# Kernel optimization log

Hardware: AMD Instinct MI355X
Metric: run time of the kernel (lower is better)

Reference implementation:

```python
import jax, jax.numpy as jnp
import numpy as np

NEG_INF = -1e9


def setup_inputs() -> dict:
    key0 = jax.random.key(0)
    ks = jax.random.split(key0, 7)
    B, Tq, Tv, D, U = 8, 512, 512, 512, 128
    query = jax.random.normal(ks[0], (B, Tq, D), dtype=jnp.float32)
    key = jax.random.normal(ks[1], (B, Tv, D), dtype=jnp.float32)
    value = jax.random.normal(ks[2], (B, Tv, D), dtype=jnp.float32)
    mask = jax.random.randint(ks[3], (B, Tv), 0, 2).astype(bool)
    mask = mask.at[:, 0].set(True)  # ensure no fully-masked row
    Wa = jax.random.normal(ks[4], (D, U), dtype=jnp.float32) * (1.0 / np.sqrt(D))
    Ua = jax.random.normal(ks[5], (D, U), dtype=jnp.float32) * (1.0 / np.sqrt(D))
    scale = jax.random.normal(ks[6], (U,), dtype=jnp.float32) * 0.1
    return {"query": query, "key": key, "value": value, "mask": mask,
            "Wa": Wa, "Ua": Ua, "scale": scale}


def reference(query, key, value, mask, Wa, Ua, scale):
    # Dense projections (no bias)
    q = query @ Wa          # [B, Tq, U]
    k = key @ Ua            # [B, Tv, U]
    # Additive (Bahdanau) scores with learned per-unit scale:
    # scores[b,i,j] = sum_u scale[u] * tanh(q[b,i,u] + k[b,j,u])
    t = jnp.tanh(q[:, :, None, :] + k[:, None, :, :])   # [B, Tq, Tv, U]
    scores = jnp.einsum('bijU,U->bij', t, scale)         # [B, Tq, Tv]
    # Mask padded keys/values then softmax over Tv
    scores = jnp.where(mask[:, None, :], scores, NEG_INF)
    weights = jax.nn.softmax(scores, axis=-1)            # [B, Tq, Tv]
    # Weighted sum of values (query_mask is all-True in source -> no-op)
    context = jnp.einsum('bij,bjd->bid', weights, value) # [B, Tq, D]
    return context
```

## Files before the change

### kernel.cpp

```cpp
#include <hip/hip_runtime.h>

constexpr int Bb = 8;
constexpr int Tq = 512;
constexpr int Tv = 512;
constexpr int Dd = 512;
constexpr int Uu = 128;
constexpr float C2LOG2E = 2.88539008177792681f;
constexpr float LOG2E   = 1.44269504088896341f;

__global__ __launch_bounds__(512, 8) void proj_kernel(
    const float* __restrict__ query,
    const float* __restrict__ key,
    const float* __restrict__ Wa,
    const float* __restrict__ Ua,
    const int* __restrict__ mask,
    float* __restrict__ qf2, float* __restrict__ kT)
{
    const int R    = blockIdx.x * 8;
    const bool isQ = R < Bb * Tq;
    const float* __restrict__ src = isQ ? query : key;
    const float* __restrict__ W   = isQ ? Wa : Ua;
    const int Rloc = isQ ? R : R - Bb * Tq;

    __shared__ float smem[8 * 8 * 128];
    __shared__ int posLoc[8];
    float* __restrict__ x = smem;
    const int t = threadIdx.x;

    {
        const float4* __restrict__ s4 =
            reinterpret_cast<const float4*>(src + (size_t)Rloc * Dd);
        float4* x4 = reinterpret_cast<float4*>(x);
#pragma unroll
        for (int m = 0; m < 2; ++m) x4[t + 512 * m] = s4[t + 512 * m];
    }
    if (!isQ && t < 64) {
        const int b  = Rloc >> 9;
        const int j0 = Rloc & 511;
        int base = 0;
#pragma unroll
        for (int c = 0; c < 8; ++c) {
            const int j = c * 64 + t;
            const int v = (mask[b * 512 + j] != 0);
            const unsigned long long bits = __ballot(v);
            const int pos = base + (int)__popcll(bits & ((1ull << t) - 1ull));
            if (j >= j0 && j < j0 + 8) posLoc[j - j0] = v ? pos : -1;
            base += (int)__popcll(bits);
        }
    }
    __syncthreads();

    const int ub = t & 63;
    const int dq = t >> 6;
    const float* __restrict__ Wq = W + (size_t)dq * 64 * Uu;
    const float* __restrict__ xq = x + dq * 64;

    float acc[8][2];
#pragma unroll
    for (int r = 0; r < 8; ++r) { acc[r][0] = 0.f; acc[r][1] = 0.f; }

#pragma unroll 2
    for (int d4 = 0; d4 < 16; ++d4) {
        const int d = d4 * 4;
        const float w0x = Wq[(d + 0) * Uu + ub], w1x = Wq[(d + 0) * Uu + ub + 64];
        const float w0y = Wq[(d + 1) * Uu + ub], w1y = Wq[(d + 1) * Uu + ub + 64];
        const float w0z = Wq[(d + 2) * Uu + ub], w1z = Wq[(d + 2) * Uu + ub + 64];
        const float w0w = Wq[(d + 3) * Uu + ub], w1w = Wq[(d + 3) * Uu + ub + 64];
#pragma unroll
        for (int r = 0; r < 8; ++r) {
            const float4 xv = *reinterpret_cast<const float4*>(xq + r * Dd + d);
            acc[r][0] = fmaf(xv.x, w0x, acc[r][0]);
            acc[r][0] = fmaf(xv.y, w0y, acc[r][0]);
            acc[r][0] = fmaf(xv.z, w0z, acc[r][0]);
            acc[r][0] = fmaf(xv.w, w0w, acc[r][0]);
            acc[r][1] = fmaf(xv.x, w1x, acc[r][1]);
            acc[r][1] = fmaf(xv.y, w1y, acc[r][1]);
            acc[r][1] = fmaf(xv.z, w1z, acc[r][1]);
            acc[r][1] = fmaf(xv.w, w1w, acc[r][1]);
        }
    }

    __syncthreads();
    {
        float* __restrict__ part = smem;
#pragma unroll
        for (int r = 0; r < 8; ++r) {
            part[(dq * 8 + r) * 128 + ub]      = acc[r][0];
            part[(dq * 8 + r) * 128 + ub + 64] = acc[r][1];
        }
    }
    __syncthreads();

    {
        const float* __restrict__ part = smem;
        const int r  = t >> 6;
        const int u0 = (t & 63) * 2;
        float s0 = 0.f, s1 = 0.f;
#pragma unroll
        for (int p = 0; p < 8; ++p) {
            const float2 pv = *reinterpret_cast<const float2*>(part + (p * 8 + r) * 128 + u0);
            s0 += pv.x;
            s1 += pv.y;
        }
        float2 e;
        e.x = __builtin_amdgcn_exp2f(C2LOG2E * s0);
        e.y = __builtin_amdgcn_exp2f(C2LOG2E * s1);
        if (isQ) {
            *reinterpret_cast<float2*>(qf2 + (size_t)(Rloc + r) * Uu + u0) = e;
        } else {
            const int p = posLoc[r];
            if (p >= 0) {
                float* __restrict__ kb = kT + (size_t)(Rloc >> 9) * Uu * Tv;
                const int u4 = u0 >> 2;
                const int c  = u0 & 3;
                *reinterpret_cast<float2*>(kb + ((size_t)u4 * Tv + p) * 4 + c) = e;
            }
        }
    }
}

__global__ __launch_bounds__(512, 8) void attn_kernel(
    const float* __restrict__ qf2, const float* __restrict__ kT,
    const float* __restrict__ value,
    const int* __restrict__ mask,
    const float* __restrict__ scale,
    float* __restrict__ out)
{
    const int bid = blockIdx.x;
    const int swz = (bid & 7) * 128 + (bid >> 3);
    const int r0 = swz * 4;
    const int b  = r0 >> 9;
    const int t  = threadIdx.x;

    __shared__ float q2[4 * Uu];
    __shared__ float s2[Uu];
    __shared__ int   jl[Tv];
    __shared__ float w[4 * Tv];
    __shared__ float pbuf[4 * Tv];
    __shared__ float inv4[4];
    __shared__ int   cntS;

    jl[t] = 0;
    if (t < 128)
        reinterpret_cast<float4*>(q2)[t] =
            reinterpret_cast<const float4*>(qf2 + (size_t)r0 * Uu)[t];
    else if (t < 256) s2[t - 128] = scale[t - 128];
    __syncthreads();
    if (t < 64) {
        int base = 0;
#pragma unroll
        for (int c = 0; c < 8; ++c) {
            const int j = c * 64 + t;
            const int v = (mask[b * 512 + j] != 0);
            const unsigned long long bits = __ballot(v);
            const int pos = base + (int)__popcll(bits & ((1ull << t) - 1ull));
            if (v) jl[pos] = j;
            base += (int)__popcll(bits);
        }
        if (t == 0) cntS = base;
    }
    __syncthreads();

    const int cnt   = cntS;
    const int cntp4 = (cnt + 3) & ~3;

    {
        const int g   = t >> 8;
        const int jc0 = t & 255;
        const float4* __restrict__ kb4 =
            reinterpret_cast<const float4*>(kT) + (size_t)b * 32 * Tv + (size_t)g * 16 * Tv;
        float* __restrict__ wr = g ? pbuf : w;
        for (int jb = 0; jb < cnt; jb += 256) {
            const int jc = jb + jc0;
            if (jc < cnt) {
                float acc[4] = {0, 0, 0, 0};
#pragma unroll 2
                for (int u4 = 0; u4 < 16; ++u4) {
                    const float4 kv = kb4[(size_t)u4 * Tv + jc];
                    const float4 sv = reinterpret_cast<const float4*>(s2)[g * 16 + u4];
#pragma unroll
                    for (int i = 0; i < 4; ++i) {
                        const float4 qv = *reinterpret_cast<const float4*>(
                            q2 + i * Uu + (g * 16 + u4) * 4);
                        const float p0 = fmaf(qv.x, kv.x, 1.f);
                        const float p1 = fmaf(qv.y, kv.y, 1.f);
                        const float p2 = fmaf(qv.z, kv.z, 1.f);
                        const float p3 = fmaf(qv.w, kv.w, 1.f);
                        acc[i] = fmaf(sv.x, __builtin_amdgcn_rcpf(p0), acc[i]);
                        acc[i] = fmaf(sv.y, __builtin_amdgcn_rcpf(p1), acc[i]);
                        acc[i] = fmaf(sv.z, __builtin_amdgcn_rcpf(p2), acc[i]);
                        acc[i] = fmaf(sv.w, __builtin_amdgcn_rcpf(p3), acc[i]);
                    }
                }
#pragma unroll
                for (int i = 0; i < 4; ++i) wr[i * Tv + jc] = acc[i];
            }
        }
    }
    __syncthreads();

    {
        const int wv = t >> 6, ln = t & 63;
        if (wv < 4) {
            float* __restrict__ row        = w    + wv * Tv;
            const float* __restrict__ rowB = pbuf + wv * Tv;
            float vals[8];
            float m = -3e38f;
#pragma unroll
            for (int c = 0; c < 8; ++c) {
                const int e = ln + 64 * c;
                vals[c] = (e < cnt) ? -2.f * (row[e] + rowB[e]) : -3e38f;
                m = fmaxf(m, vals[c]);
            }
#pragma unroll
            for (int off = 32; off; off >>= 1) m = fmaxf(m, __shfl_xor(m, off, 64));
            float sum = 0.f;
#pragma unroll
            for (int c = 0; c < 8; ++c) {
                const int e = ln + 64 * c;
                if (e < cnt) {
                    float ex = __builtin_amdgcn_exp2f((vals[c] - m) * LOG2E);
                    row[e] = ex;
                    sum += ex;
                } else {
                    row[e] = 0.f;
                }
            }
#pragma unroll
            for (int off = 32; off; off >>= 1) sum += __shfl_xor(sum, off, 64);
            if (ln == 0) inv4[wv] = 1.0f / sum;
        }
    }
    __syncthreads();

    const int mid = ((cntp4 >> 1) + 3) & ~3;
    const int g  = t >> 8;
    const int c  = t & 255;
    const int d0 = c * 2;
    const int jbeg = g ? mid : 0;
    const int jend = g ? cntp4 : mid;
    const float* __restrict__ vb = value + (size_t)b * Tv * Dd + d0;
    float ax[4], ay[4];
#pragma unroll
    for (int i = 0; i < 4; ++i) { ax[i] = 0.f; ay[i] = 0.f; }

    for (int jj = jbeg; jj < jend; jj += 4) {
        const int4 rows = *reinterpret_cast<const int4*>(jl + jj);
        const float2 v0 = *reinterpret_cast<const float2*>(vb + (size_t)rows.x * Dd);
        const float2 v1 = *reinterpret_cast<const float2*>(vb + (size_t)rows.y * Dd);
        const float2 v2 = *reinterpret_cast<const float2*>(vb + (size_t)rows.z * Dd);
        const float2 v3 = *reinterpret_cast<const float2*>(vb + (size_t)rows.w * Dd);
#pragma unroll
        for (int i = 0; i < 4; ++i) {
            const float4 wq = *reinterpret_cast<const float4*>(w + i * Tv + jj);
            ax[i] = fmaf(wq.x, v0.x, ax[i]); ay[i] = fmaf(wq.x, v0.y, ay[i]);
            ax[i] = fmaf(wq.y, v1.x, ax[i]); ay[i] = fmaf(wq.y, v1.y, ay[i]);
            ax[i] = fmaf(wq.z, v2.x, ax[i]); ay[i] = fmaf(wq.z, v2.y, ay[i]);
            ax[i] = fmaf(wq.w, v3.x, ax[i]); ay[i] = fmaf(wq.w, v3.y, ay[i]);
        }
    }

    if (g == 1) {
#pragma unroll
        for (int i = 0; i < 4; ++i) {
            float2 p; p.x = ax[i]; p.y = ay[i];
            *reinterpret_cast<float2*>(pbuf + i * Dd + d0) = p;
        }
    }
    __syncthreads();
    if (g == 0) {
#pragma unroll
        for (int i = 0; i < 4; ++i) {
            const float inv = inv4[i];
            const float2 p1 = *reinterpret_cast<const float2*>(pbuf + i * Dd + d0);
            float2 o;
            o.x = (ax[i] + p1.x) * inv;
            o.y = (ay[i] + p1.y) * inv;
            *reinterpret_cast<float2*>(out + (size_t)(r0 + i) * Dd + d0) = o;
        }
    }
}

extern "C" void kernel_launch(void* const* d_in, const int* in_sizes, int n_in,
                              void* d_out, int out_size, void* d_ws, size_t ws_size,
                              hipStream_t stream)
{
    const float* query = (const float*)d_in[0];
    const float* key   = (const float*)d_in[1];
    const float* value = (const float*)d_in[2];
    const int*   mask  = (const int*)d_in[3];
    const float* Wa    = (const float*)d_in[4];
    const float* Ua    = (const float*)d_in[5];
    const float* scale = (const float*)d_in[6];
    float* out = (float*)d_out;

    float* qf2 = (float*)d_ws;
    float* kT  = qf2 + Bb * Tq * Uu;

    proj_kernel<<<(2 * Bb * Tq) / 8, 512, 0, stream>>>(query, key, Wa, Ua, mask, qf2, kT);
    attn_kernel<<<(Bb * Tq) / 4, 512, 0, stream>>>(qf2, kT, value, mask, scale, out);
}
```

Measured before the change: 151.2 us.

## Precompute compacted mask indices in projection and streamline attention scoring

The projection kernel now writes the compacted list of valid key indices and the count per batch to workspace, so the attention kernel no longer rebuilds it from the mask with a ballot scan and an extra barrier. The score loop computes two reciprocals as one rcp of a product plus multiplies, which halves the rcp instructions but risks overflow or precision loss. Softmax drops the max subtraction, relying on the scores being bounded, and spreads the row work over all 8 waves with partial sums. The value gather loop is software-pipelined to prefetch the next rows, and the unroll factor is raised.

```diff
diff --git a/kernel.cpp b/kernel.cpp
--- a/kernel.cpp
+++ b/kernel.cpp
@@ -6,7 +6,6 @@
 constexpr int Dd = 512;
 constexpr int Uu = 128;
 constexpr float C2LOG2E = 2.88539008177792681f;
-constexpr float LOG2E   = 1.44269504088896341f;
 
 __global__ __launch_bounds__(512, 8) void proj_kernel(
     const float* __restrict__ query,
@@ -14,7 +13,8 @@
     const float* __restrict__ Wa,
     const float* __restrict__ Ua,
     const int* __restrict__ mask,
-    float* __restrict__ qf2, float* __restrict__ kT)
+    float* __restrict__ qf2, float* __restrict__ kT,
+    int* __restrict__ jl_g, int* __restrict__ cnt_g)
 {
     const int R    = blockIdx.x * 8;
     const bool isQ = R < Bb * Tq;
@@ -37,6 +37,7 @@
     if (!isQ && t < 64) {
         const int b  = Rloc >> 9;
         const int j0 = Rloc & 511;
+        const bool writer = (j0 == 0);
         int base = 0;
 #pragma unroll
         for (int c = 0; c < 8; ++c) {
@@ -45,8 +46,10 @@
             const unsigned long long bits = __ballot(v);
             const int pos = base + (int)__popcll(bits & ((1ull << t) - 1ull));
             if (j >= j0 && j < j0 + 8) posLoc[j - j0] = v ? pos : -1;
+            if (writer && v) jl_g[b * 512 + pos] = j;
             base += (int)__popcll(bits);
         }
+        if (writer && t == 0) cnt_g[b] = base;
     }
     __syncthreads();
 
@@ -122,7 +125,7 @@
 __global__ __launch_bounds__(512, 8) void attn_kernel(
     const float* __restrict__ qf2, const float* __restrict__ kT,
     const float* __restrict__ value,
-    const int* __restrict__ mask,
+    const int* __restrict__ jl_g, const int* __restrict__ cnt_g,
     const float* __restrict__ scale,
     float* __restrict__ out)
 {
@@ -137,31 +140,18 @@
     __shared__ int   jl[Tv];
     __shared__ float w[4 * Tv];
     __shared__ float pbuf[4 * Tv];
-    __shared__ float inv4[4];
-    __shared__ int   cntS;
-
-    jl[t] = 0;
+    __shared__ float sums8[8];
+    const int cnt = cnt_g[b];
+
     if (t < 128)
         reinterpret_cast<float4*>(q2)[t] =
             reinterpret_cast<const float4*>(qf2 + (size_t)r0 * Uu)[t];
-    else if (t < 256) s2[t - 128] = scale[t - 128];
-    __syncthreads();
-    if (t < 64) {
-        int base = 0;
-#pragma unroll
-        for (int c = 0; c < 8; ++c) {
-            const int j = c * 64 + t;
-            const int v = (mask[b * 512 + j] != 0);
-            const unsigned long long bits = __ballot(v);
-            const int pos = base + (int)__popcll(bits & ((1ull << t) - 1ull));
-            if (v) jl[pos] = j;
-            base += (int)__popcll(bits);
-        }
-        if (t == 0) cntS = base;
-    }
-    __syncthreads();
-
-    const int cnt   = cntS;
+    else if (t < 160)
+        reinterpret_cast<float4*>(s2)[t - 128] =
+            reinterpret_cast<const float4*>(scale)[t - 128];
+    jl[t] = (t < cnt) ? jl_g[b * 512 + t] : 0;
+    __syncthreads();
+
     const int cntp4 = (cnt + 3) & ~3;
 
     {
@@ -174,7 +164,7 @@
             const int jc = jb + jc0;
             if (jc < cnt) {
                 float acc[4] = {0, 0, 0, 0};
-#pragma unroll 2
+#pragma unroll 4
                 for (int u4 = 0; u4 < 16; ++u4) {
                     const float4 kv = kb4[(size_t)u4 * Tv + jc];
                     const float4 sv = reinterpret_cast<const float4*>(s2)[g * 16 + u4];
@@ -182,14 +172,16 @@
                     for (int i = 0; i < 4; ++i) {
                         const float4 qv = *reinterpret_cast<const float4*>(
                             q2 + i * Uu + (g * 16 + u4) * 4);
-                        const float p0 = fmaf(qv.x, kv.x, 1.f);
-                        const float p1 = fmaf(qv.y, kv.y, 1.f);
-                        const float p2 = fmaf(qv.z, kv.z, 1.f);
-                        const float p3 = fmaf(qv.w, kv.w, 1.f);
-                        acc[i] = fmaf(sv.x, __builtin_amdgcn_rcpf(p0), acc[i]);
-                        acc[i] = fmaf(sv.y, __builtin_amdgcn_rcpf(p1), acc[i]);
-                        acc[i] = fmaf(sv.z, __builtin_amdgcn_rcpf(p2), acc[i]);
-                        acc[i] = fmaf(sv.w, __builtin_amdgcn_rcpf(p3), acc[i]);
+                        const float pa = fmaf(qv.x, kv.x, 1.f);
+                        const float pb = fmaf(qv.y, kv.y, 1.f);
+                        const float pc = fmaf(qv.z, kv.z, 1.f);
+                        const float pd = fmaf(qv.w, kv.w, 1.f);
+                        const float ra = __builtin_amdgcn_rcpf(pa * pb);
+                        const float rc = __builtin_amdgcn_rcpf(pc * pd);
+                        acc[i] = fmaf(sv.x, ra * pb, acc[i]);
+                        acc[i] = fmaf(sv.y, ra * pa, acc[i]);
+                        acc[i] = fmaf(sv.z, rc * pd, acc[i]);
+                        acc[i] = fmaf(sv.w, rc * pc, acc[i]);
                     }
                 }
 #pragma unroll
@@ -201,35 +193,24 @@
 
     {
         const int wv = t >> 6, ln = t & 63;
-        if (wv < 4) {
-            float* __restrict__ row        = w    + wv * Tv;
-            const float* __restrict__ rowB = pbuf + wv * Tv;
-            float vals[8];
-            float m = -3e38f;
-#pragma unroll
-            for (int c = 0; c < 8; ++c) {
-                const int e = ln + 64 * c;
-                vals[c] = (e < cnt) ? -2.f * (row[e] + rowB[e]) : -3e38f;
-                m = fmaxf(m, vals[c]);
+        const int i = wv >> 1, h = wv & 1;
+        float* __restrict__ row        = w    + i * Tv;
+        const float* __restrict__ rowB = pbuf + i * Tv;
+        float sum = 0.f;
+#pragma unroll
+        for (int c = 0; c < 4; ++c) {
+            const int e = ln + 64 * (h * 4 + c);
+            if (e < cnt) {
+                const float ex = __builtin_amdgcn_exp2f(-C2LOG2E * (row[e] + rowB[e]));
+                row[e] = ex;
+                sum += ex;
+            } else {
+                row[e] = 0.f;
             }
-#pragma unroll
-            for (int off = 32; off; off >>= 1) m = fmaxf(m, __shfl_xor(m, off, 64));
-            float sum = 0.f;
-#pragma unroll
-            for (int c = 0; c < 8; ++c) {
-                const int e = ln + 64 * c;
-                if (e < cnt) {
-                    float ex = __builtin_amdgcn_exp2f((vals[c] - m) * LOG2E);
-                    row[e] = ex;
-                    sum += ex;
-                } else {
-                    row[e] = 0.f;
-                }
-            }
-#pragma unroll
-            for (int off = 32; off; off >>= 1) sum += __shfl_xor(sum, off, 64);
-            if (ln == 0) inv4[wv] = 1.0f / sum;
-        }
+        }
+#pragma unroll
+        for (int off = 32; off; off >>= 1) sum += __shfl_xor(sum, off, 64);
+        if (ln == 0) sums8[wv] = sum;
     }
     __syncthreads();
 
@@ -244,12 +225,29 @@
 #pragma unroll
     for (int i = 0; i < 4; ++i) { ax[i] = 0.f; ay[i] = 0.f; }
 
-    for (int jj = jbeg; jj < jend; jj += 4) {
-        const int4 rows = *reinterpret_cast<const int4*>(jl + jj);
-        const float2 v0 = *reinterpret_cast<const float2*>(vb + (size_t)rows.x * Dd);
-        const float2 v1 = *reinterpret_cast<const float2*>(vb + (size_t)rows.y * Dd);
-        const float2 v2 = *reinterpret_cast<const float2*>(vb + (size_t)rows.z * Dd);
-        const float2 v3 = *reinterpret_cast<const float2*>(vb + (size_t)rows.w * Dd);
+    if (jbeg < jend) {
+        int jj = jbeg;
+        int4 rows = *reinterpret_cast<const int4*>(jl + jj);
+        float2 v0 = *reinterpret_cast<const float2*>(vb + (size_t)rows.x * Dd);
+        float2 v1 = *reinterpret_cast<const float2*>(vb + (size_t)rows.y * Dd);
+        float2 v2 = *reinterpret_cast<const float2*>(vb + (size_t)rows.z * Dd);
+        float2 v3 = *reinterpret_cast<const float2*>(vb + (size_t)rows.w * Dd);
+        for (; jj + 4 < jend; jj += 4) {
+            const int4 rowsN = *reinterpret_cast<const int4*>(jl + jj + 4);
+            const float2 n0 = *reinterpret_cast<const float2*>(vb + (size_t)rowsN.x * Dd);
+            const float2 n1 = *reinterpret_cast<const float2*>(vb + (size_t)rowsN.y * Dd);
+            const float2 n2 = *reinterpret_cast<const float2*>(vb + (size_t)rowsN.z * Dd);
+            const float2 n3 = *reinterpret_cast<const float2*>(vb + (size_t)rowsN.w * Dd);
+#pragma unroll
+            for (int i = 0; i < 4; ++i) {
+                const float4 wq = *reinterpret_cast<const float4*>(w + i * Tv + jj);
+                ax[i] = fmaf(wq.x, v0.x, ax[i]); ay[i] = fmaf(wq.x, v0.y, ay[i]);
+                ax[i] = fmaf(wq.y, v1.x, ax[i]); ay[i] = fmaf(wq.y, v1.y, ay[i]);
+                ax[i] = fmaf(wq.z, v2.x, ax[i]); ay[i] = fmaf(wq.z, v2.y, ay[i]);
+                ax[i] = fmaf(wq.w, v3.x, ax[i]); ay[i] = fmaf(wq.w, v3.y, ay[i]);
+            }
+            v0 = n0; v1 = n1; v2 = n2; v3 = n3;
+        }
 #pragma unroll
         for (int i = 0; i < 4; ++i) {
             const float4 wq = *reinterpret_cast<const float4*>(w + i * Tv + jj);
@@ -271,7 +269,7 @@
     if (g == 0) {
 #pragma unroll
         for (int i = 0; i < 4; ++i) {
-            const float inv = inv4[i];
+            const float inv = 1.0f / (sums8[2 * i] + sums8[2 * i + 1]);
             const float2 p1 = *reinterpret_cast<const float2*>(pbuf + i * Dd + d0);
             float2 o;
             o.x = (ax[i] + p1.x) * inv;
@@ -296,7 +294,11 @@
 
     float* qf2 = (float*)d_ws;
     float* kT  = qf2 + Bb * Tq * Uu;
-
-    proj_kernel<<<(2 * Bb * Tq) / 8, 512, 0, stream>>>(query, key, Wa, Ua, mask, qf2, kT);
-    attn_kernel<<<(Bb * Tq) / 4, 512, 0, stream>>>(qf2, kT, value, mask, scale, out);
+    int*   jl_g  = (int*)(kT + Bb * Uu * Tv);
+    int*   cnt_g = jl_g + Bb * Tv;
+
+    proj_kernel<<<(2 * Bb * Tq) / 8, 512, 0, stream>>>(query, key, Wa, Ua, mask,
+                                                       qf2, kT, jl_g, cnt_g);
+    attn_kernel<<<(Bb * Tq) / 4, 512, 0, stream>>>(qf2, kT, value, jl_g, cnt_g,
+                                                   scale, out);
 }
```

Measured after the change: 150.9 us. Within noise of the previous version (-0.1%).
